# Optimization experiments

Hardware: AMD Instinct MI355X
Metric: run time of the kernel (lower is better)

## Reference

```python
import jax, jax.numpy as jnp
import numpy as np

N = 16_777_216  # point count


def _skew(v):
    zero = jnp.zeros((), v.dtype)
    return jnp.stack([
        jnp.stack([zero, -v[2], v[1]]),
        jnp.stack([v[2], zero, -v[0]]),
        jnp.stack([-v[1], v[0], zero]),
    ])


def _se3_exp(tau):
    # tau = [rho(3), theta(3)]; returns (R, t) of exp(tau^)
    rho, theta = tau[:3], tau[3:]
    W = _skew(theta)
    W2 = W @ W
    angle = jnp.linalg.norm(theta)
    small = angle < 1e-5
    a = jnp.where(small, jnp.ones((), tau.dtype), angle)  # safe divisor
    I = jnp.eye(3, dtype=tau.dtype)
    A = jnp.where(small, 1.0, jnp.sin(a) / a)                    # SO3 W coeff
    B = jnp.where(small, 0.5, (1.0 - jnp.cos(a)) / (a * a))      # SO3 W2 / V W coeff
    C = jnp.where(small, 1.0 / 6.0, (a - jnp.sin(a)) / (a ** 3)) # V W2 coeff
    R = I + A * W + B * W2
    Vm = I + B * W + C * W2
    return R, Vm @ rho


def setup_inputs() -> dict:
    key = jax.random.key(0)
    kx, kr, kt, ks = jax.random.split(key, 4)
    x = jax.random.normal(kx, (N, 4), dtype=jnp.float32)
    rot_delta = 0.1 * jax.random.normal(kr, (3,), dtype=jnp.float32)
    trans_delta = 0.1 * jax.random.normal(kt, (3,), dtype=jnp.float32)
    scale = 1.0 + 0.05 * jax.random.normal(ks, (3,), dtype=jnp.float32)
    R = jnp.eye(3, dtype=jnp.float32)
    T = jnp.zeros((3,), dtype=jnp.float32)
    return {"x": x, "rot_delta": rot_delta, "trans_delta": trans_delta,
            "scale": scale, "R": R, "T": T}


def reference(x, rot_delta, trans_delta, scale, R, T):
    tau = jnp.concatenate([trans_delta, rot_delta])  # [6]
    delta_r, delta_t = _se3_exp(tau)
    top = jnp.concatenate([scale * (delta_r @ R), (T + delta_t)[:, None]], axis=1)  # [3,4]
    bottom = jnp.array([[0.0, 0.0, 0.0, 1.0]], dtype=x.dtype)
    trans = jnp.concatenate([top, bottom], axis=0)  # [4,4]
    # y = (trans @ x.T).T == x @ trans.T
    return x @ trans.T
```

## Files before the change

kernel.cpp:

```cpp
#include <hip/hip_runtime.h>
#include <math.h>

__global__ void build_trans(const float* __restrict__ rot_delta,
                            const float* __restrict__ trans_delta,
                            const float* __restrict__ scale,
                            const float* __restrict__ Rin,
                            const float* __restrict__ Tin,
                            float* __restrict__ M) {
    if (threadIdx.x != 0 || blockIdx.x != 0) return;

    const float th0 = rot_delta[0], th1 = rot_delta[1], th2 = rot_delta[2];
    const float r0 = trans_delta[0], r1 = trans_delta[1], r2 = trans_delta[2];

    const float angle = sqrtf(th0*th0 + th1*th1 + th2*th2);
    const bool small = angle < 1e-5f;
    const float a = small ? 1.0f : angle;
    const float s = sinf(a), c = cosf(a);
    const float A = small ? 1.0f        : s / a;
    const float B = small ? 0.5f        : (1.0f - c) / (a * a);
    const float C = small ? (1.0f/6.0f) : (a - s) / (a * a * a);

    float W[3][3] = {{0.0f, -th2,  th1},
                     { th2, 0.0f, -th0},
                     {-th1,  th0, 0.0f}};
    float W2[3][3];
    for (int i = 0; i < 3; ++i)
        for (int j = 0; j < 3; ++j)
            W2[i][j] = W[i][0]*W[0][j] + W[i][1]*W[1][j] + W[i][2]*W[2][j];

    float Rd[3][3], Vm[3][3];
    for (int i = 0; i < 3; ++i)
        for (int j = 0; j < 3; ++j) {
            const float I = (i == j) ? 1.0f : 0.0f;
            Rd[i][j] = I + A * W[i][j] + B * W2[i][j];
            Vm[i][j] = I + B * W[i][j] + C * W2[i][j];
        }

    const float dt0 = Vm[0][0]*r0 + Vm[0][1]*r1 + Vm[0][2]*r2;
    const float dt1 = Vm[1][0]*r0 + Vm[1][1]*r1 + Vm[1][2]*r2;
    const float dt2 = Vm[2][0]*r0 + Vm[2][1]*r1 + Vm[2][2]*r2;

    for (int i = 0; i < 3; ++i)
        for (int j = 0; j < 3; ++j) {
            const float v = Rd[i][0]*Rin[0*3+j] + Rd[i][1]*Rin[1*3+j] + Rd[i][2]*Rin[2*3+j];
            M[i*4 + j] = scale[j] * v;
        }
    M[0*4 + 3] = Tin[0] + dt0;
    M[1*4 + 3] = Tin[1] + dt1;
    M[2*4 + 3] = Tin[2] + dt2;
    M[3*4 + 0] = 0.0f; M[3*4 + 1] = 0.0f; M[3*4 + 2] = 0.0f; M[3*4 + 3] = 1.0f;
}

__global__ __launch_bounds__(256) void apply_trans(const float4* __restrict__ x,
                                                   const float* __restrict__ M,
                                                   float4* __restrict__ out,
                                                   int n) {
    const float m00 = M[0],  m01 = M[1],  m02 = M[2],  m03 = M[3];
    const float m10 = M[4],  m11 = M[5],  m12 = M[6],  m13 = M[7];
    const float m20 = M[8],  m21 = M[9],  m22 = M[10], m23 = M[11];

    const int i = blockIdx.x * blockDim.x + threadIdx.x;
    if (i >= n) return;
    const float4 v = x[i];
    float4 o;
    o.x = fmaf(m00, v.x, fmaf(m01, v.y, fmaf(m02, v.z, m03 * v.w)));
    o.y = fmaf(m10, v.x, fmaf(m11, v.y, fmaf(m12, v.z, m13 * v.w)));
    o.z = fmaf(m20, v.x, fmaf(m21, v.y, fmaf(m22, v.z, m23 * v.w)));
    o.w = v.w;
    out[i] = o;
}

extern "C" void kernel_launch(void* const* d_in, const int* in_sizes, int n_in,
                              void* d_out, int out_size, void* d_ws, size_t ws_size,
                              hipStream_t stream) {
    const float* x          = (const float*)d_in[0];
    const float* rot_delta  = (const float*)d_in[1];
    const float* trans_delta= (const float*)d_in[2];
    const float* scale      = (const float*)d_in[3];
    const float* R          = (const float*)d_in[4];
    const float* T          = (const float*)d_in[5];
    float* M = (float*)d_ws;

    build_trans<<<1, 64, 0, stream>>>(rot_delta, trans_delta, scale, R, T, M);

    const int n = in_sizes[0] / 4;
    const int block = 256;
    const int grid = (n + block - 1) / block;
    apply_trans<<<grid, block, 0, stream>>>((const float4*)x, M, (float4*)d_out, n);
}
```

Before: 427.9 us.

## Fuse transform build into apply kernel and use nontemporal loads/stores

Removes the separate single-thread build kernel. Thread 0 of every block now recomputes the 3x4 transform into shared memory, with a block barrier before use. Streaming loads and stores switch to nontemporal builtins to reduce cache pollution. The trade-off is that each of the 65k blocks pays for the serial transcendental setup and a __syncthreads, which may stall the memory stream at block start.

```diff
diff --git a/kernel.cpp b/kernel.cpp
--- a/kernel.cpp
+++ b/kernel.cpp
@@ -1,90 +1,91 @@
 #include <hip/hip_runtime.h>
 #include <math.h>
 
-__global__ void build_trans(const float* __restrict__ rot_delta,
-                            const float* __restrict__ trans_delta,
-                            const float* __restrict__ scale,
-                            const float* __restrict__ Rin,
-                            const float* __restrict__ Tin,
-                            float* __restrict__ M) {
-    if (threadIdx.x != 0 || blockIdx.x != 0) return;
+typedef float v4f __attribute__((ext_vector_type(4)));
 
-    const float th0 = rot_delta[0], th1 = rot_delta[1], th2 = rot_delta[2];
-    const float r0 = trans_delta[0], r1 = trans_delta[1], r2 = trans_delta[2];
+__global__ __launch_bounds__(256) void srt_fused(const v4f* __restrict__ x,
+                                                 v4f* __restrict__ out,
+                                                 int n,
+                                                 const float* __restrict__ rot_delta,
+                                                 const float* __restrict__ trans_delta,
+                                                 const float* __restrict__ scale,
+                                                 const float* __restrict__ Rin,
+                                                 const float* __restrict__ Tin) {
+    __shared__ float Ms[12];
 
-    const float angle = sqrtf(th0*th0 + th1*th1 + th2*th2);
-    const bool small = angle < 1e-5f;
-    const float a = small ? 1.0f : angle;
-    const float s = sinf(a), c = cosf(a);
-    const float A = small ? 1.0f        : s / a;
-    const float B = small ? 0.5f        : (1.0f - c) / (a * a);
-    const float C = small ? (1.0f/6.0f) : (a - s) / (a * a * a);
+    if (threadIdx.x == 0) {
+        const float th0 = rot_delta[0], th1 = rot_delta[1], th2 = rot_delta[2];
+        const float r0 = trans_delta[0], r1 = trans_delta[1], r2 = trans_delta[2];
 
-    float W[3][3] = {{0.0f, -th2,  th1},
-                     { th2, 0.0f, -th0},
-                     {-th1,  th0, 0.0f}};
-    float W2[3][3];
-    for (int i = 0; i < 3; ++i)
-        for (int j = 0; j < 3; ++j)
-            W2[i][j] = W[i][0]*W[0][j] + W[i][1]*W[1][j] + W[i][2]*W[2][j];
+        const float angle = sqrtf(th0*th0 + th1*th1 + th2*th2);
+        const bool small = angle < 1e-5f;
+        const float a = small ? 1.0f : angle;
+        const float s = sinf(a), c = cosf(a);
+        const float A = small ? 1.0f        : s / a;
+        const float B = small ? 0.5f        : (1.0f - c) / (a * a);
+        const float C = small ? (1.0f/6.0f) : (a - s) / (a * a * a);
 
-    float Rd[3][3], Vm[3][3];
-    for (int i = 0; i < 3; ++i)
-        for (int j = 0; j < 3; ++j) {
-            const float I = (i == j) ? 1.0f : 0.0f;
-            Rd[i][j] = I + A * W[i][j] + B * W2[i][j];
-            Vm[i][j] = I + B * W[i][j] + C * W2[i][j];
+        float W[3][3] = {{0.0f, -th2,  th1},
+                         { th2, 0.0f, -th0},
+                         {-th1,  th0, 0.0f}};
+        float W2[3][3];
+        for (int i = 0; i < 3; ++i)
+            for (int j = 0; j < 3; ++j)
+                W2[i][j] = W[i][0]*W[0][j] + W[i][1]*W[1][j] + W[i][2]*W[2][j];
+
+        float Rd[3][3], Vm[3][3];
+        for (int i = 0; i < 3; ++i)
+            for (int j = 0; j < 3; ++j) {
+                const float I = (i == j) ? 1.0f : 0.0f;
+                Rd[i][j] = I + A * W[i][j] + B * W2[i][j];
+                Vm[i][j] = I + B * W[i][j] + C * W2[i][j];
+            }
+
+        const float dt0 = Vm[0][0]*r0 + Vm[0][1]*r1 + Vm[0][2]*r2;
+        const float dt1 = Vm[1][0]*r0 + Vm[1][1]*r1 + Vm[1][2]*r2;
+        const float dt2 = Vm[2][0]*r0 + Vm[2][1]*r1 + Vm[2][2]*r2;
+
+        for (int i = 0; i < 3; ++i) {
+            for (int j = 0; j < 3; ++j) {
+                const float v = Rd[i][0]*Rin[0*3+j] + Rd[i][1]*Rin[1*3+j] + Rd[i][2]*Rin[2*3+j];
+                Ms[i*4 + j] = scale[j] * v;
+            }
         }
+        Ms[0*4 + 3] = Tin[0] + dt0;
+        Ms[1*4 + 3] = Tin[1] + dt1;
+        Ms[2*4 + 3] = Tin[2] + dt2;
+    }
+    __syncthreads();
 
-    const float dt0 = Vm[0][0]*r0 + Vm[0][1]*r1 + Vm[0][2]*r2;
-    const float dt1 = Vm[1][0]*r0 + Vm[1][1]*r1 + Vm[1][2]*r2;
-    const float dt2 = Vm[2][0]*r0 + Vm[2][1]*r1 + Vm[2][2]*r2;
-
-    for (int i = 0; i < 3; ++i)
-        for (int j = 0; j < 3; ++j) {
-            const float v = Rd[i][0]*Rin[0*3+j] + Rd[i][1]*Rin[1*3+j] + Rd[i][2]*Rin[2*3+j];
-            M[i*4 + j] = scale[j] * v;
-        }
-    M[0*4 + 3] = Tin[0] + dt0;
-    M[1*4 + 3] = Tin[1] + dt1;
-    M[2*4 + 3] = Tin[2] + dt2;
-    M[3*4 + 0] = 0.0f; M[3*4 + 1] = 0.0f; M[3*4 + 2] = 0.0f; M[3*4 + 3] = 1.0f;
-}
-
-__global__ __launch_bounds__(256) void apply_trans(const float4* __restrict__ x,
-                                                   const float* __restrict__ M,
-                                                   float4* __restrict__ out,
-                                                   int n) {
-    const float m00 = M[0],  m01 = M[1],  m02 = M[2],  m03 = M[3];
-    const float m10 = M[4],  m11 = M[5],  m12 = M[6],  m13 = M[7];
-    const float m20 = M[8],  m21 = M[9],  m22 = M[10], m23 = M[11];
+    const float m00 = Ms[0], m01 = Ms[1], m02 = Ms[2],  m03 = Ms[3];
+    const float m10 = Ms[4], m11 = Ms[5], m12 = Ms[6],  m13 = Ms[7];
+    const float m20 = Ms[8], m21 = Ms[9], m22 = Ms[10], m23 = Ms[11];
 
     const int i = blockIdx.x * blockDim.x + threadIdx.x;
     if (i >= n) return;
-    const float4 v = x[i];
-    float4 o;
+
+    const v4f v = __builtin_nontemporal_load(x + i);
+    v4f o;
     o.x = fmaf(m00, v.x, fmaf(m01, v.y, fmaf(m02, v.z, m03 * v.w)));
     o.y = fmaf(m10, v.x, fmaf(m11, v.y, fmaf(m12, v.z, m13 * v.w)));
     o.z = fmaf(m20, v.x, fmaf(m21, v.y, fmaf(m22, v.z, m23 * v.w)));
     o.w = v.w;
-    out[i] = o;
+    __builtin_nontemporal_store(o, out + i);
 }
 
 extern "C" void kernel_launch(void* const* d_in, const int* in_sizes, int n_in,
                               void* d_out, int out_size, void* d_ws, size_t ws_size,
                               hipStream_t stream) {
-    const float* x          = (const float*)d_in[0];
-    const float* rot_delta  = (const float*)d_in[1];
-    const float* trans_delta= (const float*)d_in[2];
-    const float* scale      = (const float*)d_in[3];
-    const float* R          = (const float*)d_in[4];
-    const float* T          = (const float*)d_in[5];
-    float* M = (float*)d_ws;
-
-    build_trans<<<1, 64, 0, stream>>>(rot_delta, trans_delta, scale, R, T, M);
+    const float* x           = (const float*)d_in[0];
+    const float* rot_delta   = (const float*)d_in[1];
+    const float* trans_delta = (const float*)d_in[2];
+    const float* scale       = (const float*)d_in[3];
+    const float* R           = (const float*)d_in[4];
+    const float* T           = (const float*)d_in[5];
 
     const int n = in_sizes[0] / 4;
     const int block = 256;
     const int grid = (n + block - 1) / block;
-    apply_trans<<<grid, block, 0, stream>>>((const float4*)x, M, (float4*)d_out, n);
+    srt_fused<<<grid, block, 0, stream>>>((const v4f*)x, (v4f*)d_out, n,
+                                          rot_delta, trans_delta, scale, R, T);
 }
```

Measured after the change: 437.5 us. +2.3%, slower.
